# Performance work log

Hardware: AMD Instinct MI355X
Metric: run time of the kernel (lower is better)

Reference implementation:

```python
import jax, jax.numpy as jnp
import numpy as np

D_MODEL = 256; N_HEADS = 8; N_LEVELS = 4; N_POINTS = 4
D_HEAD = D_MODEL // N_HEADS


def setup_inputs() -> dict:
    key = jax.random.key(0)
    ks = jax.random.split(key, 8)
    N, Lq = 4, 4096
    shapes = np.array([4096, 2048, 1024, 512], dtype=np.int32)  # temporal lengths per level
    Len_in = int(shapes.sum())  # 7680
    start = np.concatenate([[0], np.cumsum(shapes)[:-1]]).astype(np.int32)
    HLP = N_HEADS * N_LEVELS * N_POINTS
    return {
        "query": jax.random.normal(ks[0], (N, Lq, D_MODEL), jnp.float32),
        "reference_points": jax.random.uniform(ks[1], (N, Lq, N_LEVELS, 1), jnp.float32),
        "input_flatten": jax.random.normal(ks[2], (N, Len_in, D_MODEL), jnp.float32),
        "input_spatial_shapes": jnp.asarray(shapes),
        "input_level_start_index": jnp.asarray(start),
        "W_off": jax.random.normal(ks[3], (D_MODEL, HLP), jnp.float32) * 0.01,
        "b_off": jax.random.normal(ks[4], (HLP,), jnp.float32) * 2.0,
        "W_aw": jax.random.normal(ks[5], (D_MODEL, HLP), jnp.float32) * 0.02,
        "b_aw": jnp.zeros((HLP,), jnp.float32),
        "W_v": jax.random.normal(ks[6], (D_MODEL, D_MODEL), jnp.float32) / np.sqrt(D_MODEL).astype(np.float32),
        "b_v": jnp.zeros((D_MODEL,), jnp.float32),
        "W_out": jax.random.normal(ks[7], (D_MODEL, D_MODEL), jnp.float32) / np.sqrt(D_MODEL).astype(np.float32),
        "b_out": jnp.zeros((D_MODEL,), jnp.float32),
    }


def reference(query, reference_points, input_flatten, input_spatial_shapes,
              input_level_start_index, W_off, b_off, W_aw, b_aw, W_v, b_v,
              W_out, b_out):
    N, Lq, C = query.shape
    M, L, P, Dh = N_HEADS, N_LEVELS, N_POINTS, D_HEAD
    S = input_flatten.shape[1]

    value = (input_flatten @ W_v + b_v).reshape(N, S, M, Dh)
    off = (query @ W_off + b_off).reshape(N, Lq, M, L, P)
    aw = jax.nn.softmax((query @ W_aw + b_aw).reshape(N, Lq, M, L * P), axis=-1)
    aw = aw.reshape(N, Lq, M, L, P)

    # reference_points last dim == 1 branch: loc = ref + off / T_l, in [0,1]
    T = input_spatial_shapes.astype(jnp.float32)[None, None, None, :, None]  # [1,1,1,L,1]
    loc = reference_points[:, :, None, :, None, 0] + off / T  # [N,Lq,M,L,P]

    # grid_sample(align_corners=False, padding_mode='border') along W with H=1, y=0.5:
    # pixel coord x = loc*T - 0.5, clamped to [0, T-1], then linear interp.
    x = jnp.clip(loc * T - 0.5, 0.0, T - 1.0)
    x0 = jnp.floor(x)
    w1 = x - x0                                   # frac weight for right neighbor
    i0 = x0.astype(jnp.int32)
    i1 = jnp.minimum(i0 + 1, input_spatial_shapes[None, None, None, :, None] - 1)
    base = input_level_start_index[None, None, None, :, None]
    g0 = i0 + base                                # global flattened indices [N,Lq,M,L,P]
    g1 = i1 + base

    v = value.transpose(0, 2, 1, 3)               # [N,M,S,Dh]

    def gather(idx):
        idxt = idx.transpose(0, 2, 1, 3, 4).reshape(N, M, Lq * L * P, 1)
        return jnp.take_along_axis(v, idxt, axis=2).reshape(N, M, Lq, L, P, Dh)

    s0 = gather(g0)
    s1 = gather(g1)
    w1t = w1.transpose(0, 2, 1, 3, 4)[..., None]   # [N,M,Lq,L,P,1]
    samp = s0 * (1.0 - w1t) + s1 * w1t             # [N,M,Lq,L,P,Dh]

    awt = aw.transpose(0, 2, 1, 3, 4)[..., None]
    out = (samp * awt).sum(axis=(3, 4))            # [N,M,Lq,Dh]
    out = out.transpose(0, 2, 1, 3).reshape(N, Lq, M * Dh)
    return out @ W_out + b_out
```

## Files before the change

kernel.cpp:

```cpp
#include <hip/hip_runtime.h>
#include <hip/hip_bf16.h>
#include <cstddef>
#include <cstdint>

#define D_MODEL   256
#define N_HEADS   8
#define N_LEVELS  4
#define N_POINTS  4
#define D_HEAD    32
#define HLP       128
#define NBATCH    4
#define LQ        4096
#define S_LEN     7680

typedef __attribute__((ext_vector_type(8))) short  short8;
typedef __attribute__((ext_vector_type(4))) float  f32x4;
typedef __attribute__((ext_vector_type(8))) unsigned short ushort8;

__device__ __forceinline__ unsigned short f2bf(float x) {
    __hip_bfloat16 h = __float2bfloat16(x);
    return *reinterpret_cast<unsigned short*>(&h);
}
__device__ __forceinline__ float bf2f(unsigned short u) {
    unsigned int v = ((unsigned int)u) << 16;
    return *reinterpret_cast<float*>(&v);
}

__device__ __forceinline__ void gload_lds16(const void* g, void* l) {
    __builtin_amdgcn_global_load_lds(
        (const __attribute__((address_space(1))) void*)g,
        (__attribute__((address_space(3))) void*)l,
        16, 0, 0);
}

__global__ __launch_bounds__(256) void prep_kernel(
    const float* __restrict__ W_v,  const float* __restrict__ W_off,
    const float* __restrict__ W_aw, const float* __restrict__ W_out,
    const float* __restrict__ b_off, const float* __restrict__ b_aw,
    unsigned short* __restrict__ Wv_t, unsigned short* __restrict__ Wcat_t,
    unsigned short* __restrict__ Wout_t, float* __restrict__ bcat)
{
    __shared__ float t[64][65];
    const int z   = blockIdx.z;
    const int k0  = blockIdx.y * 64;
    const int n0  = blockIdx.x * 64;
    const int tid = threadIdx.x;

    const float* src; int srcN; int cs; unsigned short* dst;
    if (z == 0)      { src = W_v;   srcN = 256; cs = n0;       dst = Wv_t;  }
    else if (z == 2) { src = W_out; srcN = 256; cs = n0;       dst = Wout_t;}
    else if (n0 < 128){ src = W_off; srcN = 128; cs = n0;      dst = Wcat_t;}
    else             { src = W_aw;  srcN = 128; cs = n0 - 128; dst = Wcat_t;}

    #pragma unroll
    for (int i = 0; i < 16; ++i) {
        int idx = tid + i * 256;
        int kk = idx >> 6, nn = idx & 63;
        t[kk][nn] = src[(size_t)(k0 + kk) * srcN + cs + nn];
    }
    __syncthreads();
    #pragma unroll
    for (int i = 0; i < 16; ++i) {
        int idx = tid + i * 256;
        int nn = idx >> 6, kk = idx & 63;
        dst[(size_t)(n0 + nn) * 256 + k0 + kk] = f2bf(t[kk][nn]);
    }
    if (z == 1 && blockIdx.x == 0 && blockIdx.y == 0) {
        bcat[tid] = (tid < 128) ? b_off[tid] : b_aw[tid - 128];
    }
}

template <bool A_FP32, bool BF16_OUT>
__global__ __launch_bounds__(256) void mfma_gemm_kernel(
    const void* __restrict__ Aptr,
    const unsigned short* __restrict__ Bt,
    const float* __restrict__ bias,
    void* __restrict__ Cout, int M)
{
    __shared__ alignas(16) unsigned short Als[8][64][8];
    __shared__ alignas(16) unsigned short Bls[8][64][8];

    const int tid  = threadIdx.x;
    const int lane = tid & 63;
    const int w    = tid >> 6;
    const int wm   = w & 1;
    const int wn   = w >> 1;
    const int row0 = blockIdx.y * 128;
    const int col0 = blockIdx.x * 128;

    const int lr = (lane & 15);
    const int lk = (lane >> 4) * 8;

    f32x4 acc[4][4] = {};

    for (int kt = 0; kt < 8; ++kt) {
        const int k0 = kt * 32;
        #pragma unroll
        for (int c = 0; c < 2; ++c) {
            const int im = w * 2 + c;
            if (A_FP32) {
                const float* Af = (const float*)Aptr;
                const float* ap = Af + (size_t)(row0 + im * 16 + lr) * 256 + k0 + lk;
                const float4 a0 = *(const float4*)(ap);
                const float4 a1 = *(const float4*)(ap + 4);
                short8 pk;
                pk[0] = (short)f2bf(a0.x); pk[1] = (short)f2bf(a0.y);
                pk[2] = (short)f2bf(a0.z); pk[3] = (short)f2bf(a0.w);
                pk[4] = (short)f2bf(a1.x); pk[5] = (short)f2bf(a1.y);
                pk[6] = (short)f2bf(a1.z); pk[7] = (short)f2bf(a1.w);
                *(short8*)&Als[im][lane][0] = pk;
            } else {
                const unsigned short* Ab = (const unsigned short*)Aptr;
                const size_t ga = (size_t)(row0 + im * 16 + lr) * 256 + k0 + lk;
                gload_lds16(Ab + ga, &Als[im][0][0]);
            }
            const size_t gb = (size_t)(col0 + im * 16 + lr) * 256 + k0 + lk;
            gload_lds16(Bt + gb, &Bls[im][0][0]);
        }
        __syncthreads();

        short8 af[4], bfr[4];
        #pragma unroll
        for (int i = 0; i < 4; ++i) af[i]  = *(const short8*)&Als[wm * 4 + i][lane][0];
        #pragma unroll
        for (int j = 0; j < 4; ++j) bfr[j] = *(const short8*)&Bls[wn * 4 + j][lane][0];

        #pragma unroll
        for (int i = 0; i < 4; ++i)
            #pragma unroll
            for (int j = 0; j < 4; ++j)
                acc[i][j] = __builtin_amdgcn_mfma_f32_16x16x32_bf16(
                    af[i], bfr[j], acc[i][j], 0, 0, 0);
        __syncthreads();
    }

    const int r0 = row0 + wm * 64;
    const int c0 = col0 + wn * 64;
    const int prow = (lane >> 4) * 4;
    const int pcol = lane & 15;
    #pragma unroll
    for (int j = 0; j < 4; ++j) {
        const int col = c0 + j * 16 + pcol;
        const float bs = bias[col];
        #pragma unroll
        for (int i = 0; i < 4; ++i) {
            #pragma unroll
            for (int r = 0; r < 4; ++r) {
                const int row = r0 + i * 16 + prow + r;
                const float v = acc[i][j][r] + bs;
                if (BF16_OUT)
                    ((unsigned short*)Cout)[(size_t)row * 256 + col] = f2bf(v);
                else
                    ((float*)Cout)[(size_t)row * 256 + col] = v;
            }
        }
    }
}

__global__ __launch_bounds__(256) void sample_kernel(
    const float* __restrict__ P, const float* __restrict__ refp,
    const int* __restrict__ shapes, const int* __restrict__ lstart,
    const unsigned short* __restrict__ value, unsigned short* __restrict__ tout)
{
    __shared__ int   sG0[8][HLP];
    __shared__ int   sG1[8][HLP];
    __shared__ float sW [8][HLP];
    __shared__ float sA [8][HLP];

    const int b    = blockIdx.x;
    const int xcd  = b & 7;
    const int slot = b >> 3;
    const int n    = xcd >> 1;
    const int qg   = (slot << 1) | (xcd & 1);
    const int nq0  = n * LQ + qg * 8;
    const int tid  = threadIdx.x;

    #pragma unroll
    for (int i = 0; i < 4; ++i) {
        const int idx = tid + i * 256;
        const int q   = idx >> 7;
        const int j   = idx & 127;
        const int l   = (j >> 2) & 3;
        const int nq  = nq0 + q;
        const float off   = P[(size_t)nq * 256 + j];
        const float logit = P[(size_t)nq * 256 + 128 + j];
        const float T     = (float)shapes[l];
        const float ref   = refp[(size_t)nq * N_LEVELS + l];
        float x = ref * T + off - 0.5f;
        x = fminf(fmaxf(x, 0.0f), T - 1.0f);
        const float x0 = floorf(x);
        const int   i0 = (int)x0;
        const int   i1 = min(i0 + 1, shapes[l] - 1);
        const int   base = lstart[l];
        sG0[q][j] = i0 + base;
        sG1[q][j] = i1 + base;
        sW [q][j] = x - x0;
        sA [q][j] = logit;
    }
    __syncthreads();

    if (tid < 64) {
        const int q = tid >> 3;
        const int m = tid & 7;
        float e[16];
        float mx = -1e30f;
        #pragma unroll
        for (int i = 0; i < 16; ++i) { e[i] = sA[q][m * 16 + i]; mx = fmaxf(mx, e[i]); }
        float s = 0.f;
        #pragma unroll
        for (int i = 0; i < 16; ++i) { e[i] = __expf(e[i] - mx); s += e[i]; }
        const float rs = 1.0f / s;
        #pragma unroll
        for (int i = 0; i < 16; ++i) sA[q][m * 16 + i] = e[i] * rs;
    }
    __syncthreads();

    const int q  = tid >> 5;
    const int r  = tid & 31;
    const int m  = r >> 2;
    const int ql = r & 3;
    const unsigned short* vb = value + (size_t)n * S_LEN * 256 + m * 32 + ql * 8;

    float acc[8] = {};
    #pragma unroll
    for (int i = 0; i < 16; ++i) {
        const int j = m * 16 + i;
        const float a  = sA[q][j];
        const float ww = sW[q][j];
        const ushort8 u0 = *(const ushort8*)(vb + (size_t)sG0[q][j] * 256);
        const ushort8 u1 = *(const ushort8*)(vb + (size_t)sG1[q][j] * 256);
        #pragma unroll
        for (int d = 0; d < 8; ++d) {
            const float v0 = bf2f(u0[d]);
            const float v1 = bf2f(u1[d]);
            acc[d] += a * (v0 + ww * (v1 - v0));
        }
    }
    ushort8 o;
    #pragma unroll
    for (int d = 0; d < 8; ++d) o[d] = f2bf(acc[d]);
    *(ushort8*)(tout + (size_t)(nq0 + q) * 256 + r * 8) = o;
}

extern "C" void kernel_launch(void* const* d_in, const int* in_sizes, int n_in,
                              void* d_out, int out_size, void* d_ws, size_t ws_size,
                              hipStream_t stream)
{
    const float* query  = (const float*)d_in[0];
    const float* refp   = (const float*)d_in[1];
    const float* inflat = (const float*)d_in[2];
    const int*   shapes = (const int*)d_in[3];
    const int*   lstart = (const int*)d_in[4];
    const float* W_off  = (const float*)d_in[5];
    const float* b_off  = (const float*)d_in[6];
    const float* W_aw   = (const float*)d_in[7];
    const float* b_aw   = (const float*)d_in[8];
    const float* W_v    = (const float*)d_in[9];
    const float* b_v    = (const float*)d_in[10];
    const float* W_out  = (const float*)d_in[11];
    const float* b_out  = (const float*)d_in[12];

    const int M_val = NBATCH * S_LEN;
    const int M_q   = NBATCH * LQ;

    char* p = (char*)d_ws;
    unsigned short* value_bf = (unsigned short*)p; p += (size_t)M_val * D_MODEL * 2;
    float*          P        = (float*)p;          p += (size_t)M_q * 256 * 4;
    unsigned short* tbuf     = (unsigned short*)p; p += (size_t)M_q * D_MODEL * 2;
    unsigned short* Wv_t     = (unsigned short*)p; p += 256 * 256 * 2;
    unsigned short* Wcat_t   = (unsigned short*)p; p += 256 * 256 * 2;
    unsigned short* Wout_t   = (unsigned short*)p; p += 256 * 256 * 2;
    float*          bcat     = (float*)p;          p += 256 * 4;

    prep_kernel<<<dim3(4, 4, 3), 256, 0, stream>>>(
        W_v, W_off, W_aw, W_out, b_off, b_aw, Wv_t, Wcat_t, Wout_t, bcat);
    mfma_gemm_kernel<true, true><<<dim3(2, M_val / 128), 256, 0, stream>>>(
        inflat, Wv_t, b_v, value_bf, M_val);
    mfma_gemm_kernel<true, false><<<dim3(2, M_q / 128), 256, 0, stream>>>(
        query, Wcat_t, bcat, P, M_q);
    sample_kernel<<<M_q / 8, 256, 0, stream>>>(
        P, refp, shapes, lstart, value_bf, tbuf);
    mfma_gemm_kernel<false, false><<<dim3(2, M_q / 128), 256, 0, stream>>>(
        tbuf, Wout_t, b_out, (float*)d_out, M_q);
}
```

Baseline: 173.7 us.

## Merge value and query GEMMs, split value by head-group for L2-local sampling

```diff
diff --git a/kernel.cpp b/kernel.cpp
--- a/kernel.cpp
+++ b/kernel.cpp
@@ -70,12 +70,110 @@
     }
 }
 
-template <bool A_FP32, bool BF16_OUT>
-__global__ __launch_bounds__(256) void mfma_gemm_kernel(
-    const void* __restrict__ Aptr,
+__global__ __launch_bounds__(256) void gemm_vp_kernel(
+    const float* __restrict__ inflat, const float* __restrict__ query,
+    const unsigned short* __restrict__ Wv_t, const unsigned short* __restrict__ Wcat_t,
+    const float* __restrict__ b_v, const float* __restrict__ bcat,
+    unsigned short* __restrict__ value2, float* __restrict__ P)
+{
+    __shared__ alignas(16) unsigned short Als[8][64][8];
+    __shared__ alignas(16) unsigned short Bls[8][64][8];
+
+    const int job = blockIdx.x;
+    const bool is_val = (job < 480);
+    const int jj   = is_val ? job : (job - 480);
+    const int row0 = (jj >> 1) * 128;
+    const int col0 = (jj & 1) * 128;
+    const float* A = is_val ? inflat : query;
+    const unsigned short* Bt = is_val ? Wv_t : Wcat_t;
+    const float* bias = is_val ? b_v : bcat;
+
+    const int tid  = threadIdx.x;
+    const int lane = tid & 63;
+    const int w    = tid >> 6;
+    const int wm   = w & 1;
+    const int wn   = w >> 1;
+    const int lr   = lane & 15;
+    const int lk   = (lane >> 4) * 8;
+
+    f32x4 acc[4][4] = {};
+
+    for (int kt = 0; kt < 8; ++kt) {
+        const int k0 = kt * 32;
+        #pragma unroll
+        for (int c = 0; c < 2; ++c) {
+            const int im = w * 2 + c;
+            const float* ap = A + (size_t)(row0 + im * 16 + lr) * 256 + k0 + lk;
+            const float4 a0 = *(const float4*)(ap);
+            const float4 a1 = *(const float4*)(ap + 4);
+            short8 pk;
+            pk[0] = (short)f2bf(a0.x); pk[1] = (short)f2bf(a0.y);
+            pk[2] = (short)f2bf(a0.z); pk[3] = (short)f2bf(a0.w);
+            pk[4] = (short)f2bf(a1.x); pk[5] = (short)f2bf(a1.y);
+            pk[6] = (short)f2bf(a1.z); pk[7] = (short)f2bf(a1.w);
+            *(short8*)&Als[im][lane][0] = pk;
+            const size_t gb = (size_t)(col0 + im * 16 + lr) * 256 + k0 + lk;
+            gload_lds16(Bt + gb, &Bls[im][0][0]);
+        }
+        __syncthreads();
+
+        short8 af[4], bfr[4];
+        #pragma unroll
+        for (int i = 0; i < 4; ++i) af[i]  = *(const short8*)&Als[wm * 4 + i][lane][0];
+        #pragma unroll
+        for (int j = 0; j < 4; ++j) bfr[j] = *(const short8*)&Bls[wn * 4 + j][lane][0];
+
+        #pragma unroll
+        for (int i = 0; i < 4; ++i)
+            #pragma unroll
+            for (int j = 0; j < 4; ++j)
+                acc[i][j] = __builtin_amdgcn_mfma_f32_16x16x32_bf16(
+                    af[i], bfr[j], acc[i][j], 0, 0, 0);
+        __syncthreads();
+    }
+
+    const int prow = (lane >> 4) * 4;
+    const int pcol = lane & 15;
+    if (is_val) {
+        const int n  = row0 / S_LEN;
+        const int s0 = row0 - n * S_LEN;
+        const int gg = col0 >> 7;
+        unsigned short* dst = value2 + ((size_t)(n * 2 + gg) * S_LEN + s0) * 128;
+        #pragma unroll
+        for (int j = 0; j < 4; ++j) {
+            const int inner = wn * 64 + j * 16 + pcol;
+            const float bs = bias[col0 + inner];
+            #pragma unroll
+            for (int i = 0; i < 4; ++i) {
+                #pragma unroll
+                for (int r = 0; r < 4; ++r) {
+                    const int rl = wm * 64 + i * 16 + prow + r;
+                    dst[(size_t)rl * 128 + inner] = f2bf(acc[i][j][r] + bs);
+                }
+            }
+        }
+    } else {
+        #pragma unroll
+        for (int j = 0; j < 4; ++j) {
+            const int col = col0 + wn * 64 + j * 16 + pcol;
+            const float bs = bias[col];
+            #pragma unroll
+            for (int i = 0; i < 4; ++i) {
+                #pragma unroll
+                for (int r = 0; r < 4; ++r) {
+                    const int row = row0 + wm * 64 + i * 16 + prow + r;
+                    P[(size_t)row * 256 + col] = acc[i][j][r] + bs;
+                }
+            }
+        }
+    }
+}
+
+__global__ __launch_bounds__(256) void gemm_out_kernel(
+    const unsigned short* __restrict__ A,
     const unsigned short* __restrict__ Bt,
     const float* __restrict__ bias,
-    void* __restrict__ Cout, int M)
+    float* __restrict__ Cout)
 {
     __shared__ alignas(16) unsigned short Als[8][64][8];
     __shared__ alignas(16) unsigned short Bls[8][64][8];
@@ -87,9 +185,8 @@
     const int wn   = w >> 1;
     const int row0 = blockIdx.y * 128;
     const int col0 = blockIdx.x * 128;
-
-    const int lr = (lane & 15);
-    const int lk = (lane >> 4) * 8;
+    const int lr   = lane & 15;
+    const int lk   = (lane >> 4) * 8;
 
     f32x4 acc[4][4] = {};
 
@@ -98,24 +195,8 @@
         #pragma unroll
         for (int c = 0; c < 2; ++c) {
             const int im = w * 2 + c;
-            if (A_FP32) {
-                const float* Af = (const float*)Aptr;
-                const float* ap = Af + (size_t)(row0 + im * 16 + lr) * 256 + k0 + lk;
-                const float4 a0 = *(const float4*)(ap);
-                const float4 a1 = *(const float4*)(ap + 4);
-                short8 pk;
-                pk[0] = (short)f2bf(a0.x); pk[1] = (short)f2bf(a0.y);
-                pk[2] = (short)f2bf(a0.z); pk[3] = (short)f2bf(a0.w);
-                pk[4] = (short)f2bf(a1.x); pk[5] = (short)f2bf(a1.y);
-                pk[6] = (short)f2bf(a1.z); pk[7] = (short)f2bf(a1.w);
-                *(short8*)&Als[im][lane][0] = pk;
-            } else {
-                const unsigned short* Ab = (const unsigned short*)Aptr;
-                const size_t ga = (size_t)(row0 + im * 16 + lr) * 256 + k0 + lk;
-                gload_lds16(Ab + ga, &Als[im][0][0]);
-            }
-            const size_t gb = (size_t)(col0 + im * 16 + lr) * 256 + k0 + lk;
-            gload_lds16(Bt + gb, &Bls[im][0][0]);
+            gload_lds16(A + (size_t)(row0 + im * 16 + lr) * 256 + k0 + lk, &Als[im][0][0]);
+            gload_lds16(Bt + (size_t)(col0 + im * 16 + lr) * 256 + k0 + lk, &Bls[im][0][0]);
         }
         __syncthreads();
 
@@ -134,24 +215,18 @@
         __syncthreads();
     }
 
-    const int r0 = row0 + wm * 64;
-    const int c0 = col0 + wn * 64;
     const int prow = (lane >> 4) * 4;
     const int pcol = lane & 15;
     #pragma unroll
     for (int j = 0; j < 4; ++j) {
-        const int col = c0 + j * 16 + pcol;
+        const int col = col0 + wn * 64 + j * 16 + pcol;
         const float bs = bias[col];
         #pragma unroll
         for (int i = 0; i < 4; ++i) {
             #pragma unroll
             for (int r = 0; r < 4; ++r) {
-                const int row = r0 + i * 16 + prow + r;
-                const float v = acc[i][j][r] + bs;
-                if (BF16_OUT)
-                    ((unsigned short*)Cout)[(size_t)row * 256 + col] = f2bf(v);
-                else
-                    ((float*)Cout)[(size_t)row * 256 + col] = v;
+                const int row = row0 + wm * 64 + i * 16 + prow + r;
+                Cout[(size_t)row * 256 + col] = acc[i][j][r] + bs;
             }
         }
     }
@@ -160,75 +235,78 @@
 __global__ __launch_bounds__(256) void sample_kernel(
     const float* __restrict__ P, const float* __restrict__ refp,
     const int* __restrict__ shapes, const int* __restrict__ lstart,
-    const unsigned short* __restrict__ value, unsigned short* __restrict__ tout)
-{
-    __shared__ int   sG0[8][HLP];
-    __shared__ int   sG1[8][HLP];
-    __shared__ float sW [8][HLP];
-    __shared__ float sA [8][HLP];
-
-    const int b    = blockIdx.x;
-    const int xcd  = b & 7;
-    const int slot = b >> 3;
-    const int n    = xcd >> 1;
-    const int qg   = (slot << 1) | (xcd & 1);
-    const int nq0  = n * LQ + qg * 8;
-    const int tid  = threadIdx.x;
-
-    #pragma unroll
-    for (int i = 0; i < 4; ++i) {
-        const int idx = tid + i * 256;
-        const int q   = idx >> 7;
-        const int j   = idx & 127;
-        const int l   = (j >> 2) & 3;
+    const unsigned short* __restrict__ value2, unsigned short* __restrict__ tout)
+{
+    __shared__ int   sG0[16][65];
+    __shared__ int   sG1[16][65];
+    __shared__ float sW [16][65];
+    __shared__ float sA [16][65];
+
+    const int b   = blockIdx.x;
+    const int xcd = b & 7;
+    const int n   = xcd >> 1;
+    const int g   = xcd & 1;
+    const int q0  = (b >> 3) * 16;
+    const int nq0 = n * LQ + q0;
+    const int tid = threadIdx.x;
+
+    #pragma unroll
+    for (int it = 0; it < 4; ++it) {
+        const int idx = tid + it * 256;
+        const int q   = idx >> 6;
+        const int jl  = idx & 63;
+        const int l   = (jl >> 2) & 3;
+        const int jg  = g * 64 + jl;
         const int nq  = nq0 + q;
-        const float off   = P[(size_t)nq * 256 + j];
-        const float logit = P[(size_t)nq * 256 + 128 + j];
-        const float T     = (float)shapes[l];
-        const float ref   = refp[(size_t)nq * N_LEVELS + l];
+        const float off   = __builtin_nontemporal_load(P + (size_t)nq * 256 + jg);
+        const float logit = __builtin_nontemporal_load(P + (size_t)nq * 256 + 128 + jg);
+        const float ref   = __builtin_nontemporal_load(refp + (size_t)nq * N_LEVELS + l);
+        const int   sh    = shapes[l];
+        const float T     = (float)sh;
         float x = ref * T + off - 0.5f;
         x = fminf(fmaxf(x, 0.0f), T - 1.0f);
         const float x0 = floorf(x);
         const int   i0 = (int)x0;
-        const int   i1 = min(i0 + 1, shapes[l] - 1);
+        const int   i1 = min(i0 + 1, sh - 1);
         const int   base = lstart[l];
-        sG0[q][j] = i0 + base;
-        sG1[q][j] = i1 + base;
-        sW [q][j] = x - x0;
-        sA [q][j] = logit;
+        sG0[q][jl] = i0 + base;
+        sG1[q][jl] = i1 + base;
+        sW [q][jl] = x - x0;
+        sA [q][jl] = logit;
     }
     __syncthreads();
 
     if (tid < 64) {
-        const int q = tid >> 3;
-        const int m = tid & 7;
+        const int q  = tid >> 2;
+        const int mh = tid & 3;
         float e[16];
         float mx = -1e30f;
         #pragma unroll
-        for (int i = 0; i < 16; ++i) { e[i] = sA[q][m * 16 + i]; mx = fmaxf(mx, e[i]); }
+        for (int i = 0; i < 16; ++i) { e[i] = sA[q][mh * 16 + i]; mx = fmaxf(mx, e[i]); }
         float s = 0.f;
         #pragma unroll
         for (int i = 0; i < 16; ++i) { e[i] = __expf(e[i] - mx); s += e[i]; }
         const float rs = 1.0f / s;
         #pragma unroll
-        for (int i = 0; i < 16; ++i) sA[q][m * 16 + i] = e[i] * rs;
+        for (int i = 0; i < 16; ++i) sA[q][mh * 16 + i] = e[i] * rs;
     }
     __syncthreads();
 
-    const int q  = tid >> 5;
-    const int r  = tid & 31;
-    const int m  = r >> 2;
+    const int q  = tid >> 4;
+    const int r  = tid & 15;
+    const int mh = r >> 2;
     const int ql = r & 3;
-    const unsigned short* vb = value + (size_t)n * S_LEN * 256 + m * 32 + ql * 8;
+    const unsigned short* vb =
+        value2 + (size_t)xcd * S_LEN * 128 + mh * 32 + ql * 8;
 
     float acc[8] = {};
     #pragma unroll
     for (int i = 0; i < 16; ++i) {
-        const int j = m * 16 + i;
+        const int j = mh * 16 + i;
         const float a  = sA[q][j];
         const float ww = sW[q][j];
-        const ushort8 u0 = *(const ushort8*)(vb + (size_t)sG0[q][j] * 256);
-        const ushort8 u1 = *(const ushort8*)(vb + (size_t)sG1[q][j] * 256);
+        const ushort8 u0 = *(const ushort8*)(vb + (size_t)sG0[q][j] * 128);
+        const ushort8 u1 = *(const ushort8*)(vb + (size_t)sG1[q][j] * 128);
         #pragma unroll
         for (int d = 0; d < 8; ++d) {
             const float v0 = bf2f(u0[d]);
@@ -239,7 +317,8 @@
     ushort8 o;
     #pragma unroll
     for (int d = 0; d < 8; ++d) o[d] = f2bf(acc[d]);
-    *(ushort8*)(tout + (size_t)(nq0 + q) * 256 + r * 8) = o;
+    __builtin_nontemporal_store(o,
+        (ushort8*)(tout + (size_t)(nq0 + q) * 256 + g * 128 + mh * 32 + ql * 8));
 }
 
 extern "C" void kernel_launch(void* const* d_in, const int* in_sizes, int n_in,
@@ -264,22 +343,20 @@
     const int M_q   = NBATCH * LQ;
 
     char* p = (char*)d_ws;
-    unsigned short* value_bf = (unsigned short*)p; p += (size_t)M_val * D_MODEL * 2;
-    float*          P        = (float*)p;          p += (size_t)M_q * 256 * 4;
-    unsigned short* tbuf     = (unsigned short*)p; p += (size_t)M_q * D_MODEL * 2;
-    unsigned short* Wv_t     = (unsigned short*)p; p += 256 * 256 * 2;
-    unsigned short* Wcat_t   = (unsigned short*)p; p += 256 * 256 * 2;
-    unsigned short* Wout_t   = (unsigned short*)p; p += 256 * 256 * 2;
-    float*          bcat     = (float*)p;          p += 256 * 4;
+    unsigned short* value2 = (unsigned short*)p; p += (size_t)M_val * D_MODEL * 2;
+    float*          P      = (float*)p;          p += (size_t)M_q * 256 * 4;
+    unsigned short* tbuf   = (unsigned short*)p; p += (size_t)M_q * D_MODEL * 2;
+    unsigned short* Wv_t   = (unsigned short*)p; p += 256 * 256 * 2;
+    unsigned short* Wcat_t = (unsigned short*)p; p += 256 * 256 * 2;
+    unsigned short* Wout_t = (unsigned short*)p; p += 256 * 256 * 2;
+    float*          bcat   = (float*)p;          p += 256 * 4;
 
     prep_kernel<<<dim3(4, 4, 3), 256, 0, stream>>>(
         W_v, W_off, W_aw, W_out, b_off, b_aw, Wv_t, Wcat_t, Wout_t, bcat);
-    mfma_gemm_kernel<true, true><<<dim3(2, M_val / 128), 256, 0, stream>>>(
-        inflat, Wv_t, b_v, value_bf, M_val);
-    mfma_gemm_kernel<true, false><<<dim3(2, M_q / 128), 256, 0, stream>>>(
-        query, Wcat_t, bcat, P, M_q);
-    sample_kernel<<<M_q / 8, 256, 0, stream>>>(
-        P, refp, shapes, lstart, value_bf, tbuf);
-    mfma_gemm_kernel<false, false><<<dim3(2, M_q / 128), 256, 0, stream>>>(
-        tbuf, Wout_t, b_out, (float*)d_out, M_q);
-}
+    gemm_vp_kernel<<<736, 256, 0, stream>>>(
+        inflat, query, Wv_t, Wcat_t, b_v, bcat, value2, P);
+    sample_kernel<<<2048, 256, 0, stream>>>(
+        P, refp, shapes, lstart, value2, tbuf);
+    gemm_out_kernel<<<dim3(2, M_q / 128), 256, 0, stream>>>(
+        tbuf, Wout_t, b_out, (float*)d_out);
+}
```

Result: faster. 162.2 us (-6.6%).
